# Optimization experiments

Measured on AMD Instinct MI355X. Metric: run time of the kernel, lower is better.

## Reference

```python
import jax, jax.numpy as jnp
import numpy as np
from jax import lax

ALPHA = 0.5       # DYS step size (init kwarg alpha)
SV_THRESH = 1e-6  # pinv singular-value threshold (init kwarg sv_thresh)
TOL = 1e-2        # convergence tolerance (forward default tol=0.01)


def _build_matrices(A):
    # A: (batch, m, n).  Standard-form matrix A_std = [A, -A, I_m]: (batch, m, N), N = 2n+m.
    batch, m, n = A.shape
    I_m = jnp.eye(m, dtype=A.dtype)
    A_std = jnp.concatenate([A, -A, jnp.broadcast_to(I_m, (batch, m, m))], axis=2)
    # M maps z -> u: (n, N) = [I_n, -I_n, 0]
    M = jnp.concatenate([jnp.eye(n, dtype=A.dtype), -jnp.eye(n, dtype=A.dtype),
                         jnp.zeros((n, m), dtype=A.dtype)], axis=1)
    AAt = A_std @ jnp.swapaxes(A_std, -2, -1)              # (batch, m, m)
    U, S, _ = jnp.linalg.svd(AAt)
    S_inv = jnp.where(S > SV_THRESH, 1.0 / S, jnp.zeros_like(S))
    AAt_pinv = (U * S_inv[..., None, :]) @ jnp.swapaxes(U, -2, -1)
    P_perp = jnp.swapaxes(A_std, -2, -1) @ AAt_pinv        # (batch, N, m)
    return A_std, M, P_perp


def _apply_T(z, u_nom, A_std, M, P_perp, b2):
    # One Davis-Yin splitting step. z: (batch, N), b2: (batch, m)
    x = jnp.maximum(z, 0.0)                                # proj_C2
    grad = (x @ M.T - u_nom) @ M                           # (batch, N)
    v = 2.0 * x - z - ALPHA * grad
    resid = jnp.einsum('bmN,bN->bm', A_std, v) - b2
    y = v - jnp.einsum('bNm,bm->bN', P_perp, resid)        # proj_C1
    return z + y - x


def setup_inputs() -> dict:
    key = jax.random.key(0)
    k1, k2, k3 = jax.random.split(key, 3)
    batch, m, n = 8192, 32, 16
    u_nom = jax.random.normal(k1, (batch, n), dtype=jnp.float32)
    A = jax.random.normal(k2, (batch, m, n), dtype=jnp.float32)
    b = jax.random.uniform(k3, (batch, m, 1), dtype=jnp.float32)
    return {"u_nom": u_nom, "A": A, "b": b, "max_iter": 100}


def reference(u_nom, A, b, max_iter):
    A_std, M, P_perp = _build_matrices(A)
    b2 = b[..., 0]
    batch = u_nom.shape[0]
    N = M.shape[1]
    z0 = jnp.zeros((batch, N), dtype=u_nom.dtype)

    # JFB: run to convergence (max_iter-1 steps, on-device residual check) ...
    def cond(state):
        k, z, res = state
        return jnp.logical_and(res >= TOL, k < max_iter - 1)

    def body(state):
        k, z, _ = state
        z_new = _apply_T(z, u_nom, A_std, M, P_perp, b2)
        return k + 1, z_new, jnp.max(jnp.abs(z_new - z))

    _, z, _ = lax.while_loop(cond, body, (0, z0, jnp.array(jnp.inf, dtype=u_nom.dtype)))

    # ... then one final T step (n_grad_iters=1)
    z_star = _apply_T(z, u_nom, A_std, M, P_perp, b2)
    u_star = z_star @ M.T
    return u_star, z_star
```

## Files before the change

### kernel.cpp

```cpp
#include <hip/hip_runtime.h>
#include <stdint.h>

#define TOL 1e-2f
#define WPB 4
#define WS_CTL_OFF 192
#define WS_Z_OFF   4096

#define LDSW 768

__device__ __forceinline__ float bcastf(float v, int l) {
    return __int_as_float(__builtin_amdgcn_readlane(__float_as_int(v), l));
}

template <int PAT>
__device__ __forceinline__ float swz(float v) {
    return __int_as_float(__builtin_amdgcn_ds_swizzle(__float_as_int(v), PAT));
}
#define SWZ_XOR16 0x401F

template <int MODE>
__global__ __launch_bounds__(256) __attribute__((amdgpu_waves_per_eu(1)))
void dys_pass(
    const float* __restrict__ u_nom,
    const float* __restrict__ Amat,
    const float* __restrict__ bvec,
    const int*   __restrict__ mi_ptr,
    const int*   __restrict__ ctl,
    unsigned long long* __restrict__ flags,
    float*       __restrict__ zstore,
    int zcap,
    float*       __restrict__ out,
    int B)
{
    if (MODE == 1) { if (ctl[1]) return; }

    const int tid   = threadIdx.x;
    const int lane  = tid & 63;
    const int wib   = tid >> 6;
    const int elem  = blockIdx.x * WPB + wib;
    const int row32 = lane & 31;
    const int col16 = lane & 15;

    __shared__ __align__(16) float ldsT[WPB][LDSW];
    float* T = ldsT[wib];

    const float* Ab = Amat + (size_t)elem * 512 + (size_t)row32 * 16;
    float A_row[16];
    float4 a0, a1, a2, a3;
    {
        a0 = ((const float4*)Ab)[0];
        a1 = ((const float4*)Ab)[1];
        a2 = ((const float4*)Ab)[2];
        a3 = ((const float4*)Ab)[3];
        A_row[0]=a0.x;  A_row[1]=a0.y;  A_row[2]=a0.z;  A_row[3]=a0.w;
        A_row[4]=a1.x;  A_row[5]=a1.y;  A_row[6]=a1.z;  A_row[7]=a1.w;
        A_row[8]=a2.x;  A_row[9]=a2.y;  A_row[10]=a2.z; A_row[11]=a2.w;
        A_row[12]=a3.x; A_row[13]=a3.y; A_row[14]=a3.z; A_row[15]=a3.w;
    }
    if (lane < 32) {
        float4* Td = (float4*)(T + row32 * 16);
        Td[0] = a0; Td[1] = a1; Td[2] = a2; Td[3] = a3;
    }
    const float un = u_nom[(size_t)elem * 16 + col16];
    const float bv = bvec[(size_t)elem * 32 + row32];


    float P[16];
    #pragma unroll
    for (int j = 0; j < 16; ++j) P[j] = (j == col16) ? 1.f : 0.f;
    #pragma unroll
    for (int m = 0; m < 32; ++m) {
        float am  = T[m * 16 + col16];
        float am2 = am + am;
        const float4* Rm = (const float4*)(T + m * 16);
        #pragma unroll
        for (int q = 0; q < 4; ++q) {
            float4 r = Rm[q];
            P[4*q+0] = fmaf(am2, r.x, P[4*q+0]);
            P[4*q+1] = fmaf(am2, r.y, P[4*q+1]);
            P[4*q+2] = fmaf(am2, r.z, P[4*q+2]);
            P[4*q+3] = fmaf(am2, r.w, P[4*q+3]);
        }
    }

    #pragma unroll
    for (int p = 0; p < 16; ++p) {
        float piv = bcastf(P[p], p);
        float d = __builtin_amdgcn_rcpf(piv);
        d = d * (2.f - piv * d);
        float g = P[p] * d;
        g = (col16 == p) ? (1.f - d) : g;
        float negg = -g;
        #pragma unroll
        for (int j = 0; j < 16; ++j) {
            if (j == p) continue;
            float spj = bcastf(P[j], p);
            P[j] = fmaf(negg, spj, P[j]);
        }
        P[p] = (col16 == p) ? d : negg;
    }

    if (lane < 16) {
        float4* Gd = (float4*)(T + 512 + col16 * 16);
        Gd[0] = make_float4(P[0],  P[1],  P[2],  P[3]);
        Gd[1] = make_float4(P[4],  P[5],  P[6],  P[7]);
        Gd[2] = make_float4(P[8],  P[9],  P[10], P[11]);
        Gd[3] = make_float4(P[12], P[13], P[14], P[15]);
    }

    float W[48];
    #pragma unroll
    for (int k = 0; k < 16; ++k) W[k] = 0.f;
    #pragma unroll
    for (int t = 0; t < 16; ++t) {
        float at = A_row[t];
        const float4* Gt = (const float4*)(T + 512 + t * 16);
        #pragma unroll
        for (int q = 0; q < 4; ++q) {
            float4 r = Gt[q];
            W[4*q+0] = fmaf(at, r.x, W[4*q+0]);
            W[4*q+1] = fmaf(at, r.y, W[4*q+1]);
            W[4*q+2] = fmaf(at, r.z, W[4*q+2]);
            W[4*q+3] = fmaf(at, r.w, W[4*q+3]);
        }
    }

    float v[16];
    #pragma unroll
    for (int k = 0; k < 16; ++k) v[k] = (lane < 32) ? P[k] : W[k];

    if (lane < 32) {
        #pragma unroll
        for (int k = 0; k < 16; ++k)
            W[k] = fmaf(P[k], -0.5f, (k == col16) ? 0.5f : 0.f);
    }

    {
        const bool low = (lane < 32);
        #pragma unroll
        for (int m = 0; m < 32; ++m) {
            const float4* Rm = (const float4*)(T + m * 16);
            float c0 = 0.f, c1 = 0.f, c2 = 0.f, c3 = 0.f;
            #pragma unroll
            for (int q = 0; q < 4; ++q) {
                float4 r = Rm[q];
                c0 = fmaf(v[4*q+0], r.x, c0);
                c1 = fmaf(v[4*q+1], r.y, c1);
                c2 = fmaf(v[4*q+2], r.z, c2);
                c3 = fmaf(v[4*q+3], r.w, c3);
            }
            float c = (c0 + c1) + (c2 + c3);
            float dsel = (m == row32) ? 1.f : 0.f;
            float up = fmaf(-2.f, c, dsel);
            W[16 + m] = low ? c : up;
        }
    }

    float cneg;
    {
        float c0 = 0.f, c1 = 0.f;
        #pragma unroll
        for (int m = 0; m < 32; m += 2) {
            c0 = fmaf(W[16 + m], bcastf(bv, m),     c0);
            c1 = fmaf(W[17 + m], bcastf(bv, m + 1), c1);
        }
        cneg = -(c0 + c1);
    }

    const float sgn   = (lane >= 16 && lane < 32) ? 1.f : -1.f;
    const float sgn0  = (lane & 16) ? -1.f : 1.f;
    const float nun   = -un;
    const float half0 = (lane < 32) ? 0.5f : 0.f;
    const int pslot = (lane < 16) ? lane : ((lane < 32) ? (32 + lane) : (lane - 16));

    const int mi = *mi_ptr;
    const int nsteps = (MODE == 0) ? mi : ctl[0];

    const uint32_t zoff = (uint32_t)elem * 64u + (uint32_t)lane;
    float* zbase = zstore;
    const size_t zstrideE = (size_t)B * 64;

    float z = 0.f;
    unsigned long long m0 = 0ull, m1 = 0ull, b0 = 1ull, b1 = 0ull;

    const float4* Pv = (const float4*)T;

    for (int k = 1; k <= nsteps; ++k) {
        float z16 = swz<SWZ_XOR16>(z);
        float x   = fmaxf(z, 0.f);
        float x16 = fmaxf(z16, 0.f);
        float t1  = x - x16;
        float s   = (t1 - (z - z16)) + un;
        float h   = fmaf(2.f, x, -z);

        T[pslot] = (lane < 32) ? s : h;
        float ee = fmaf(sgn0, t1, nun);

        float acc0 = cneg, acc1 = 0.f, acc2 = 0.f, acc3 = 0.f;
        #pragma unroll
        for (int q = 0; q < 12; ++q) {
            float4 p = Pv[q];
            acc0 = fmaf(W[4*q+0], p.x, acc0);
            acc1 = fmaf(W[4*q+1], p.y, acc1);
            acc2 = fmaf(W[4*q+2], p.z, acc2);
            acc3 = fmaf(W[4*q+3], p.w, acc3);
        }
        float acc = (acc0 + acc1) + (acc2 + acc3);

        float t    = fmaf(half0, ee, acc);
        float znew = fmaf(sgn, t, x);

        if (MODE == 0) {
            unsigned long long cy = b0 >> 63;
            b0 <<= 1; b1 = (b1 << 1) | cy;
            unsigned long long any = __ballot(fabsf(znew - z) >= TOL);
            if (any) { m0 |= b0; m1 |= b1; }
            if (k <= zcap) { zbase[zoff] = znew; zbase += zstrideE; }
        }
        z = znew;
    }

    if (MODE == 0) {
        if (lane == 0) {
            int slot = blockIdx.x & 7;
            atomicOr(flags + 2 * slot,     m0);
            atomicOr(flags + 2 * slot + 1, m1);
        }
    } else {
        float z16b = swz<SWZ_XOR16>(z);
        if (lane < 16) out[(size_t)elem * 16 + lane] = z - z16b;
        out[(size_t)B * 16 + (size_t)elem * 64 + lane] = z;
    }
}

__global__ void dys_reduce(const int* __restrict__ mi_ptr,
                           const unsigned long long* __restrict__ flags,
                           int zcap, int* __restrict__ ctl)
{
    if (threadIdx.x != 0) return;
    unsigned long long m0 = 0ull, m1 = 0ull;
    for (int s = 0; s < 8; ++s) { m0 |= flags[2*s]; m1 |= flags[2*s+1]; }
    int mi = *mi_ptr;
    int S = mi;
    for (int k = 1; k < mi && k < 128; ++k) {
        unsigned long long bit = (k < 64) ? ((m0 >> k) & 1ull)
                                          : ((m1 >> (k - 64)) & 1ull);
        if (!bit) { S = k + 1; break; }
    }
    if (S < 1) S = 1;
    ctl[0] = S;
    ctl[1] = (S <= zcap) ? 1 : 0;
}

__global__ __launch_bounds__(256) void dys_gather(
    const int* __restrict__ ctl, const float* __restrict__ zstore,
    float* __restrict__ out, int B)
{
    if (!ctl[1]) return;
    int tid  = blockIdx.x * 256 + threadIdx.x;
    int lane = tid & 63;
    int elem = tid >> 6;
    int S = ctl[0];
    float z = zstore[(size_t)(S - 1) * B * 64 + (size_t)elem * 64 + lane];
    float z16 = swz<SWZ_XOR16>(z);
    if (lane < 16) out[(size_t)elem * 16 + lane] = z - z16;
    out[(size_t)B * 16 + (size_t)elem * 64 + lane] = z;
}

extern "C" void kernel_launch(void* const* d_in, const int* in_sizes, int n_in,
                              void* d_out, int out_size, void* d_ws, size_t ws_size,
                              hipStream_t stream) {
    (void)n_in; (void)out_size;
    const float* u_nom = (const float*)d_in[0];
    const float* Amat  = (const float*)d_in[1];
    const float* bvec  = (const float*)d_in[2];
    const int*   mi    = (const int*)d_in[3];

    const int B = in_sizes[0] / 16;

    unsigned long long* flags = (unsigned long long*)d_ws;
    int* ctl = (int*)((char*)d_ws + WS_CTL_OFF);
    float* zstore = (float*)((char*)d_ws + WS_Z_OFF);

    const size_t stepBytes = (size_t)B * 64 * sizeof(float);
    int zcap = 0;
    if (ws_size > WS_Z_OFF + stepBytes)
        zcap = (int)((ws_size - WS_Z_OFF) / stepBytes);
    if (zcap > 127) zcap = 127;

    hipMemsetAsync(d_ws, 0, 256, stream);

    const int blocks = B / WPB;
    dys_pass<0><<<blocks, 64 * WPB, 0, stream>>>(u_nom, Amat, bvec, mi, ctl,
                                                 flags, zstore, zcap, (float*)d_out, B);
    dys_reduce<<<1, 64, 0, stream>>>(mi, flags, zcap, ctl);
    dys_pass<1><<<blocks, 64 * WPB, 0, stream>>>(u_nom, Amat, bvec, mi, ctl,
                                                 flags, zstore, zcap, (float*)d_out, B);
    dys_gather<<<B * 64 / 256, 256, 0, stream>>>(ctl, zstore, (float*)d_out, B);
}
```

Measured before the change: 268.3 us.

## Replace per-step LDS round-trip with readlane broadcasts and split the store loop

The iteration loop no longer writes s/h into LDS and reads them back as float4. Each lane instead gets the 48 operands through scalar readlane broadcasts of s (lanes 0-15) and h (lanes 32-63), which removes LDS traffic and its latency from the serial loop. The loop is split so the zstore path runs without a per-step bound check, and the waves_per_eu hint changes from 1 to 8. Readlane goes through SGPRs, so 48 v_readlane ops per step may become a new serial cost, and the occupancy hint may constrain registers.

```diff
diff --git a/kernel.cpp b/kernel.cpp
--- a/kernel.cpp
+++ b/kernel.cpp
@@ -19,7 +19,7 @@
 #define SWZ_XOR16 0x401F
 
 template <int MODE>
-__global__ __launch_bounds__(256) __attribute__((amdgpu_waves_per_eu(1)))
+__global__ __launch_bounds__(256) __attribute__((amdgpu_waves_per_eu(8)))
 void dys_pass(
     const float* __restrict__ u_nom,
     const float* __restrict__ Amat,
@@ -46,20 +46,19 @@
 
     const float* Ab = Amat + (size_t)elem * 512 + (size_t)row32 * 16;
     float A_row[16];
-    float4 a0, a1, a2, a3;
     {
-        a0 = ((const float4*)Ab)[0];
-        a1 = ((const float4*)Ab)[1];
-        a2 = ((const float4*)Ab)[2];
-        a3 = ((const float4*)Ab)[3];
-        A_row[0]=a0.x;  A_row[1]=a0.y;  A_row[2]=a0.z;  A_row[3]=a0.w;
-        A_row[4]=a1.x;  A_row[5]=a1.y;  A_row[6]=a1.z;  A_row[7]=a1.w;
-        A_row[8]=a2.x;  A_row[9]=a2.y;  A_row[10]=a2.z; A_row[11]=a2.w;
-        A_row[12]=a3.x; A_row[13]=a3.y; A_row[14]=a3.z; A_row[15]=a3.w;
+        const float4* Av4 = (const float4*)Ab;
+        ((float4*)A_row)[0] = Av4[0];
+        ((float4*)A_row)[1] = Av4[1];
+        ((float4*)A_row)[2] = Av4[2];
+        ((float4*)A_row)[3] = Av4[3];
     }
     if (lane < 32) {
         float4* Td = (float4*)(T + row32 * 16);
-        Td[0] = a0; Td[1] = a1; Td[2] = a2; Td[3] = a3;
+        Td[0] = ((float4*)A_row)[0];
+        Td[1] = ((float4*)A_row)[1];
+        Td[2] = ((float4*)A_row)[2];
+        Td[3] = ((float4*)A_row)[3];
     }
     const float un = u_nom[(size_t)elem * 16 + col16];
     const float bv = bvec[(size_t)elem * 32 + row32];
@@ -125,14 +124,9 @@
         }
     }
 
-    float v[16];
-    #pragma unroll
-    for (int k = 0; k < 16; ++k) v[k] = (lane < 32) ? P[k] : W[k];
-
-    if (lane < 32) {
-        #pragma unroll
-        for (int k = 0; k < 16; ++k)
-            W[k] = fmaf(P[k], -0.5f, (k == col16) ? 0.5f : 0.f);
+    if (lane >= 32) {
+        #pragma unroll
+        for (int k = 0; k < 16; ++k) P[k] = W[k];
     }
 
     {
@@ -144,10 +138,10 @@
             #pragma unroll
             for (int q = 0; q < 4; ++q) {
                 float4 r = Rm[q];
-                c0 = fmaf(v[4*q+0], r.x, c0);
-                c1 = fmaf(v[4*q+1], r.y, c1);
-                c2 = fmaf(v[4*q+2], r.z, c2);
-                c3 = fmaf(v[4*q+3], r.w, c3);
+                c0 = fmaf(P[4*q+0], r.x, c0);
+                c1 = fmaf(P[4*q+1], r.y, c1);
+                c2 = fmaf(P[4*q+2], r.z, c2);
+                c3 = fmaf(P[4*q+3], r.w, c3);
             }
             float c = (c0 + c1) + (c2 + c3);
             float dsel = (m == row32) ? 1.f : 0.f;
@@ -156,6 +150,12 @@
         }
     }
 
+    if (lane < 32) {
+        #pragma unroll
+        for (int k = 0; k < 16; ++k)
+            W[k] = fmaf(P[k], -0.5f, (k == col16) ? 0.5f : 0.f);
+    }
+
     float cneg;
     {
         float c0 = 0.f, c1 = 0.f;
@@ -171,7 +171,6 @@
     const float sgn0  = (lane & 16) ? -1.f : 1.f;
     const float nun   = -un;
     const float half0 = (lane < 32) ? 0.5f : 0.f;
-    const int pslot = (lane < 16) ? lane : ((lane < 32) ? (32 + lane) : (lane - 16));
 
     const int mi = *mi_ptr;
     const int nsteps = (MODE == 0) ? mi : ctl[0];
@@ -183,42 +182,47 @@
     float z = 0.f;
     unsigned long long m0 = 0ull, m1 = 0ull, b0 = 1ull, b1 = 0ull;
 
-    const float4* Pv = (const float4*)T;
-
-    for (int k = 1; k <= nsteps; ++k) {
-        float z16 = swz<SWZ_XOR16>(z);
-        float x   = fmaxf(z, 0.f);
-        float x16 = fmaxf(z16, 0.f);
-        float t1  = x - x16;
-        float s   = (t1 - (z - z16)) + un;
-        float h   = fmaf(2.f, x, -z);
-
-        T[pslot] = (lane < 32) ? s : h;
-        float ee = fmaf(sgn0, t1, nun);
-
-        float acc0 = cneg, acc1 = 0.f, acc2 = 0.f, acc3 = 0.f;
-        #pragma unroll
-        for (int q = 0; q < 12; ++q) {
-            float4 p = Pv[q];
-            acc0 = fmaf(W[4*q+0], p.x, acc0);
-            acc1 = fmaf(W[4*q+1], p.y, acc1);
-            acc2 = fmaf(W[4*q+2], p.z, acc2);
-            acc3 = fmaf(W[4*q+3], p.w, acc3);
-        }
-        float acc = (acc0 + acc1) + (acc2 + acc3);
-
-        float t    = fmaf(half0, ee, acc);
-        float znew = fmaf(sgn, t, x);
-
-        if (MODE == 0) {
-            unsigned long long cy = b0 >> 63;
-            b0 <<= 1; b1 = (b1 << 1) | cy;
-            unsigned long long any = __ballot(fabsf(znew - z) >= TOL);
-            if (any) { m0 |= b0; m1 |= b1; }
-            if (k <= zcap) { zbase[zoff] = znew; zbase += zstrideE; }
-        }
-        z = znew;
-    }
+#define DYS_STEP(DO_STORE)                                                  \
+    {                                                                       \
+        float z16 = swz<SWZ_XOR16>(z);                                      \
+        float x   = fmaxf(z, 0.f);                                          \
+        float x16 = fmaxf(z16, 0.f);                                        \
+        float t1  = x - x16;                                                \
+        float s   = (t1 - (z - z16)) + un;                                  \
+        float h   = fmaf(2.f, x, -z);                                       \
+        float ee  = fmaf(sgn0, t1, nun);                                    \
+        float acc0 = cneg, acc1 = 0.f, acc2 = 0.f, acc3 = 0.f;              \
+        _Pragma("unroll")                                                   \
+        for (int q = 0; q < 4; ++q) {                                       \
+            acc0 = fmaf(W[4*q+0], bcastf(s, 4*q+0), acc0);                  \
+            acc1 = fmaf(W[4*q+1], bcastf(s, 4*q+1), acc1);                  \
+            acc2 = fmaf(W[4*q+2], bcastf(s, 4*q+2), acc2);                  \
+            acc3 = fmaf(W[4*q+3], bcastf(s, 4*q+3), acc3);                  \
+        }                                                                   \
+        _Pragma("unroll")                                                   \
+        for (int q = 0; q < 8; ++q) {                                       \
+            acc0 = fmaf(W[16+4*q+0], bcastf(h, 32+4*q+0), acc0);            \
+            acc1 = fmaf(W[16+4*q+1], bcastf(h, 32+4*q+1), acc1);            \
+            acc2 = fmaf(W[16+4*q+2], bcastf(h, 32+4*q+2), acc2);            \
+            acc3 = fmaf(W[16+4*q+3], bcastf(h, 32+4*q+3), acc3);            \
+        }                                                                   \
+        float acc = (acc0 + acc1) + (acc2 + acc3);                          \
+        float tt   = fmaf(half0, ee, acc);                                  \
+        float znew = fmaf(sgn, tt, x);                                      \
+        if (MODE == 0) {                                                    \
+            unsigned long long cy = b0 >> 63;                               \
+            b0 <<= 1; b1 = (b1 << 1) | cy;                                  \
+            unsigned long long any = __ballot(fabsf(znew - z) >= TOL);      \
+            if (any) { m0 |= b0; m1 |= b1; }                                \
+            if (DO_STORE) { zbase[zoff] = znew; zbase += zstrideE; }        \
+        }                                                                   \
+        z = znew;                                                           \
+    }
+
+    const int kz = (MODE == 0) ? (nsteps < zcap ? nsteps : zcap) : 0;
+    for (int k = 1; k <= kz; ++k) DYS_STEP(true)
+    for (int k = kz + 1; k <= nsteps; ++k) DYS_STEP(false)
+#undef DYS_STEP
 
     if (MODE == 0) {
         if (lane == 0) {
```

After: 749.5 us. 179% more time.
